# Optimization experiments

Hardware: AMD Instinct MI355X
Metric: run time of the kernel (lower is better)

Reference implementation:

```python
import jax, jax.numpy as jnp
import numpy as np

T = 16  # fixed number of timesteps in the original module


def _lin(k, out_d, in_d):
    kw, kb = jax.random.split(k)
    s = 1.0 / np.sqrt(in_d)
    W = jax.random.uniform(kw, (out_d, in_d), minval=-s, maxval=s, dtype=jnp.float32)
    b = jax.random.uniform(kb, (out_d,), minval=-s, maxval=s, dtype=jnp.float32)
    return W, b


def setup_inputs() -> dict:
    key = jax.random.key(0)
    B = 8192
    k = jax.random.split(key, 16)
    x = jax.random.normal(k[0], (T, B, 64), dtype=jnp.float32)
    cue = jax.random.uniform(k[1], (B,), dtype=jnp.float32)
    hc1 = jnp.zeros((B, 256), jnp.float32)
    hc2 = jnp.zeros((B, 256), jnp.float32)
    hc3 = jnp.zeros((B, 256), jnp.float32)
    hc4 = jnp.zeros((B, 64), jnp.float32)
    W1i, b1i = _lin(k[2], 256, 64)
    W1h, b1h = _lin(k[3], 256, 256)
    Wf1, bf1 = _lin(k[4], 256, 64)
    W1o, b1o = _lin(k[5], 64, 256)
    W2i, b2i = _lin(k[6], 256, 64)
    W2h, b2h = _lin(k[7], 256, 256)
    Wf2, bf2 = _lin(k[8], 256, 64)
    W2o, b2o = _lin(k[9], 64, 256)
    W3i, b3i = _lin(k[10], 256, 130)
    W3h, b3h = _lin(k[11], 256, 256)
    W3o, b3o = _lin(k[12], 64, 256)
    Wfc, bfc = _lin(k[13], 2, 64)
    return dict(x=x, cue=cue, hc1=hc1, hc2=hc2, hc3=hc3, hc4=hc4,
                W1i=W1i, b1i=b1i, W1h=W1h, b1h=b1h, Wf1=Wf1, bf1=bf1, W1o=W1o, b1o=b1o,
                W2i=W2i, b2i=b2i, W2h=W2h, b2h=b2h, Wf2=Wf2, bf2=bf2, W2o=W2o, b2o=b2o,
                W3i=W3i, b3i=b3i, W3h=W3h, b3h=b3h, W3o=W3o, b3o=b3o, Wfc=Wfc, bfc=bfc)


def reference(x, cue, hc1, hc2, hc3, hc4,
              W1i, b1i, W1h, b1h, Wf1, bf1, W1o, b1o,
              W2i, b2i, W2h, b2h, Wf2, bf2, W2o, b2o,
              W3i, b3i, W3h, b3h, W3o, b3o, Wfc, bfc):
    B = x.shape[1]
    # cue row is the same at every timestep: [B, 2]
    cue_row = jnp.stack([cue * 10.0, 10.0 * jnp.abs(cue - 1.0)], axis=-1)

    def step(carry, xi):
        h1, h2, h3, h4 = carry
        # RNN stack 1 with feedback from hc4
        feed1 = h4 @ Wf1.T + bf1                                    # [B,256] (pre-tanh, stored)
        h1n = jnp.tanh(xi @ W1i.T + b1i + h1 @ W1h.T + b1h + jnp.tanh(feed1))
        out1 = jnp.tanh(h1n @ W1o.T + b1o)                           # [B,64]
        # RNN stack 2 with feedback from hc4
        feed2 = h4 @ Wf2.T + bf2
        h2n = jnp.tanh(xi @ W2i.T + b2i + h2 @ W2h.T + b2h + jnp.tanh(feed2))
        out2 = jnp.tanh(h2n @ W2o.T + b2o)                           # [B,64]
        # RNN stack 3 over concat(cue, out1, out2): [B,130]
        mid = jnp.concatenate([cue_row, out1, out2], axis=-1)
        h3n = jnp.tanh(mid @ W3i.T + b3i + h3 @ W3h.T + b3h)
        o = h3n @ W3o.T + b3o                                        # [B,64]; becomes next hc4
        of = jax.nn.relu(o)
        outf = of @ Wfc.T + bfc                                      # [B,2]
        return (h1n, h2n, h3n, o), (outf, out1, out2, feed1, feed2, of)

    (h1, h2, h3, h4), (oseq, o1, o2, f1, f2, ofa) = jax.lax.scan(
        step, (hc1, hc2, hc3, hc4), x)
    cue_arr = jnp.broadcast_to(cue_row[None, :, :], (T, B, 2))
    return (oseq, h1, h2, h3, h4, o1, o2, cue_arr, f1, f2, ofa)
```

## Files before the change

kernel.cpp:

```cpp
#include <hip/hip_runtime.h>

typedef unsigned short ushort_t;
typedef __attribute__((ext_vector_type(8))) __bf16 bf8v;
typedef __attribute__((ext_vector_type(4))) float f4v;
typedef __attribute__((ext_vector_type(4))) unsigned short us4v;

#define MFMA(a, b, c) __builtin_amdgcn_mfma_f32_16x16x32_bf16((a), (b), (c), 0, 0, 0)

#define B_TOT 8192
#define T_STEPS 16
#define M_TILE 32
#define LDH 264
#define LDS_SM 72
#define LDMID 168

#define OW1I 0
#define OW1H 16384
#define OWF1 81920
#define OW1O 98304
#define OW2I 114688
#define OW2H 131072
#define OWF2 196608
#define OW2O 212992
#define OW3I 229376
#define OW3H 270336
#define OW3O 335872
#define OWFC 352256
#define WS_TOTAL 353280

#define O_OSEQ 0
#define O_H1   262144
#define O_H2   2359296
#define O_H3   4456448
#define O_H4   6553600
#define O_O1   7077888
#define O_O2   15466496
#define O_CUE  23855104
#define O_F1   24117248
#define O_F2   57671680
#define O_OFA  91226112

__device__ __forceinline__ ushort_t f2bf(float f) {
  union { float f; unsigned u; } v; v.f = f;
  unsigned r = v.u + 0x7fffu + ((v.u >> 16) & 1u);
  return (ushort_t)(r >> 16);
}

__device__ __forceinline__ float fast_tanh(float x) {
  float e = __expf(2.0f * x);
  return 1.0f - 2.0f * __builtin_amdgcn_rcpf(e + 1.0f);
}

__device__ __forceinline__ void store_bf4(ushort_t* p, f4v v) {
  us4v q;
  q[0] = f2bf(v[0]); q[1] = f2bf(v[1]); q[2] = f2bf(v[2]); q[3] = f2bf(v[3]);
  *(us4v*)p = q;
}

__global__ void prep_kernel(const float* __restrict__ W1i, const float* __restrict__ W1h,
                            const float* __restrict__ Wf1, const float* __restrict__ W1o,
                            const float* __restrict__ W2i, const float* __restrict__ W2h,
                            const float* __restrict__ Wf2, const float* __restrict__ W2o,
                            const float* __restrict__ W3i, const float* __restrict__ W3h,
                            const float* __restrict__ W3o, const float* __restrict__ Wfc,
                            ushort_t* __restrict__ ws) {
  int i = blockIdx.x * blockDim.x + threadIdx.x;
  if (i >= WS_TOTAL) return;
  float v;
  if (i < OW1H)       v = W1i[i - OW1I];
  else if (i < OWF1)  v = W1h[i - OW1H];
  else if (i < OW1O)  v = Wf1[i - OWF1];
  else if (i < OW2I)  v = W1o[i - OW1O];
  else if (i < OW2H)  v = W2i[i - OW2I];
  else if (i < OWF2)  v = W2h[i - OW2H];
  else if (i < OW2O)  v = Wf2[i - OWF2];
  else if (i < OW3I)  v = W2o[i - OW2O];
  else if (i < OW3H) {
    int idx = i - OW3I; int j = idx / 160; int k = idx - j * 160;
    if (k < 64)       v = W3i[j * 130 + 2 + k];
    else if (k < 128) v = W3i[j * 130 + 66 + (k - 64)];
    else if (k < 130) v = W3i[j * 130 + (k - 128)];
    else              v = 0.0f;
  }
  else if (i < OW3O)  v = W3h[i - OW3H];
  else if (i < OWFC)  v = W3o[i - OW3O];
  else {
    int idx = i - OWFC; int j = idx / 64; int k = idx - j * 64;
    v = (j < 2) ? Wfc[j * 64 + k] : 0.0f;
  }
  ws[i] = f2bf(v);
}

__launch_bounds__(512)
__global__ void rnn_kernel(const float* __restrict__ x, const float* __restrict__ cue,
                           const float* __restrict__ hc1, const float* __restrict__ hc2,
                           const float* __restrict__ hc3, const float* __restrict__ hc4,
                           const float* __restrict__ b1i, const float* __restrict__ b1h,
                           const float* __restrict__ bf1p, const float* __restrict__ b1o,
                           const float* __restrict__ b2i, const float* __restrict__ b2h,
                           const float* __restrict__ bf2p, const float* __restrict__ b2o,
                           const float* __restrict__ b3i, const float* __restrict__ b3h,
                           const float* __restrict__ b3o, const float* __restrict__ bfc,
                           const ushort_t* __restrict__ ws, float* __restrict__ out) {
  __shared__ ushort_t hs1[M_TILE * LDH], hs2[M_TILE * LDH], hs3[M_TILE * LDH];
  __shared__ ushort_t h4s[M_TILE * LDS_SM], xs[M_TILE * LDS_SM], ofs[M_TILE * LDS_SM];
  __shared__ ushort_t mid[M_TILE * LDMID];

  const int tid  = threadIdx.x;
  const int m0   = blockIdx.x * M_TILE;
  const int lane = tid & 63;
  const int w    = tid >> 6;
  const int ln   = lane & 15;
  const int quad = lane >> 4;
  const int koff = quad * 8;
  const int jt0  = 2 * w;

  for (int i = tid; i < M_TILE * 256; i += 512) {
    int m = i >> 8, j = i & 255;
    hs1[m * LDH + j] = f2bf(hc1[(m0 + m) * 256 + j]);
    hs2[m * LDH + j] = f2bf(hc2[(m0 + m) * 256 + j]);
    hs3[m * LDH + j] = f2bf(hc3[(m0 + m) * 256 + j]);
  }
  for (int i = tid; i < M_TILE * 64; i += 512) {
    int m = i >> 6, j = i & 63;
    h4s[m * LDS_SM + j] = f2bf(hc4[(m0 + m) * 64 + j]);
  }
  for (int i = tid; i < M_TILE * LDMID; i += 512) mid[i] = 0;
  {
    int t = tid >> 5, r = tid & 31;
    float c = cue[m0 + r];
    float* oc = out + O_CUE + ((size_t)t * B_TOT + m0 + r) * 2;
    oc[0] = c * 10.0f;
    oc[1] = 10.0f * fabsf(c - 1.0f);
  }
  __syncthreads();
  if (tid < M_TILE) {
    float c = cue[m0 + tid];
    mid[tid * LDMID + 128] = f2bf(c * 10.0f);
    mid[tid * LDMID + 129] = f2bf(10.0f * fabsf(c - 1.0f));
  }

  f4v bf1v[2], bf2v[2], bih1v[2], bih2v[2], b3shv[2];
#pragma unroll
  for (int i = 0; i < 2; ++i) {
    int j0 = (jt0 + i) * 16 + quad * 4;
#pragma unroll
    for (int r = 0; r < 4; ++r) {
      bf1v[i][r]  = bf1p[j0 + r];
      bf2v[i][r]  = bf2p[j0 + r];
      bih1v[i][r] = b1i[j0 + r] + b1h[j0 + r];
      bih2v[i][r] = b2i[j0 + r] + b2h[j0 + r];
      b3shv[i][r] = b3i[j0 + r] + b3h[j0 + r];
    }
  }
  const int jto3 = w & 3;
  const int j0o3 = jto3 * 16 + quad * 4;
  const bool isOut2 = (w >= 4);
  f4v bo3v;
#pragma unroll
  for (int r = 0; r < 4; ++r) bo3v[r] = isOut2 ? b2o[j0o3 + r] : b1o[j0o3 + r];
  const int jto5 = w >> 1;
  const int j0o5 = jto5 * 16 + quad * 4;
  const int mo5  = (w & 1) * 16 + ln;
  f4v b3ov;
#pragma unroll
  for (int r = 0; r < 4; ++r) b3ov[r] = b3o[j0o5 + r];
  const float bfcv0 = bfc[0], bfcv1 = bfc[1];

  __syncthreads();

  f4v acc1[2][2], acc2[2][2], acc3[2][2];

  for (int t = 0; t < T_STEPS; ++t) {
    {
      int r = tid >> 4, c4 = (tid & 15) * 4;
      const float* xp = x + ((size_t)t * B_TOT + m0 + r) * 64 + c4;
      f4v xv = *(const f4v*)xp;
      store_bf4(&xs[r * LDS_SM + c4], xv);
    }
    {
      f4v aF1[2][2], aF2[2][2];
#pragma unroll
      for (int i = 0; i < 2; ++i) {
#pragma unroll
        for (int mt = 0; mt < 2; ++mt) { aF1[i][mt] = bf1v[i]; aF2[i][mt] = bf2v[i]; }
      }
#pragma unroll
      for (int kk = 0; kk < 64; kk += 32) {
        bf8v b0 = *(const bf8v*)&h4s[ln * LDS_SM + kk + koff];
        bf8v b1 = *(const bf8v*)&h4s[(16 + ln) * LDS_SM + kk + koff];
#pragma unroll
        for (int i = 0; i < 2; ++i) {
          const int ar = ((jt0 + i) * 16 + ln) * 64 + kk + koff;
          bf8v a1 = *(const bf8v*)&ws[OWF1 + ar];
          bf8v a2 = *(const bf8v*)&ws[OWF2 + ar];
          aF1[i][0] = MFMA(a1, b0, aF1[i][0]);
          aF1[i][1] = MFMA(a1, b1, aF1[i][1]);
          aF2[i][0] = MFMA(a2, b0, aF2[i][0]);
          aF2[i][1] = MFMA(a2, b1, aF2[i][1]);
        }
      }
#pragma unroll
      for (int i = 0; i < 2; ++i) {
#pragma unroll
        for (int mt = 0; mt < 2; ++mt) {
          int j0 = (jt0 + i) * 16 + quad * 4;
          int m  = mt * 16 + ln;
          size_t rowoff = ((size_t)t * B_TOT + m0 + m) * 256 + j0;
          *(f4v*)(out + O_F1 + rowoff) = aF1[i][mt];
          *(f4v*)(out + O_F2 + rowoff) = aF2[i][mt];
          f4v t1, t2;
#pragma unroll
          for (int r = 0; r < 4; ++r) {
            t1[r] = fast_tanh(aF1[i][mt][r]) + bih1v[i][r];
            t2[r] = fast_tanh(aF2[i][mt][r]) + bih2v[i][r];
          }
          acc1[i][mt] = t1; acc2[i][mt] = t2; acc3[i][mt] = b3shv[i];
        }
      }
    }
    __syncthreads();

#pragma unroll
    for (int kk = 0; kk < 64; kk += 32) {
      bf8v b0 = *(const bf8v*)&xs[ln * LDS_SM + kk + koff];
      bf8v b1 = *(const bf8v*)&xs[(16 + ln) * LDS_SM + kk + koff];
#pragma unroll
      for (int i = 0; i < 2; ++i) {
        const int ar = ((jt0 + i) * 16 + ln) * 64 + kk + koff;
        bf8v a1 = *(const bf8v*)&ws[OW1I + ar];
        bf8v a2 = *(const bf8v*)&ws[OW2I + ar];
        acc1[i][0] = MFMA(a1, b0, acc1[i][0]);
        acc1[i][1] = MFMA(a1, b1, acc1[i][1]);
        acc2[i][0] = MFMA(a2, b0, acc2[i][0]);
        acc2[i][1] = MFMA(a2, b1, acc2[i][1]);
      }
    }
#pragma unroll
    for (int kk = 0; kk < 256; kk += 32) {
      bf8v q1a = *(const bf8v*)&hs1[ln * LDH + kk + koff];
      bf8v q1b = *(const bf8v*)&hs1[(16 + ln) * LDH + kk + koff];
      bf8v q2a = *(const bf8v*)&hs2[ln * LDH + kk + koff];
      bf8v q2b = *(const bf8v*)&hs2[(16 + ln) * LDH + kk + koff];
      bf8v q3a = *(const bf8v*)&hs3[ln * LDH + kk + koff];
      bf8v q3b = *(const bf8v*)&hs3[(16 + ln) * LDH + kk + koff];
#pragma unroll
      for (int i = 0; i < 2; ++i) {
        const int ar = ((jt0 + i) * 16 + ln) * 256 + kk + koff;
        bf8v a1 = *(const bf8v*)&ws[OW1H + ar];
        bf8v a2 = *(const bf8v*)&ws[OW2H + ar];
        bf8v a3 = *(const bf8v*)&ws[OW3H + ar];
        acc1[i][0] = MFMA(a1, q1a, acc1[i][0]);
        acc1[i][1] = MFMA(a1, q1b, acc1[i][1]);
        acc2[i][0] = MFMA(a2, q2a, acc2[i][0]);
        acc2[i][1] = MFMA(a2, q2b, acc2[i][1]);
        acc3[i][0] = MFMA(a3, q3a, acc3[i][0]);
        acc3[i][1] = MFMA(a3, q3b, acc3[i][1]);
      }
    }
#pragma unroll
    for (int i = 0; i < 2; ++i) {
#pragma unroll
      for (int mt = 0; mt < 2; ++mt) {
#pragma unroll
        for (int r = 0; r < 4; ++r) {
          acc1[i][mt][r] = fast_tanh(acc1[i][mt][r]);
          acc2[i][mt][r] = fast_tanh(acc2[i][mt][r]);
        }
      }
    }
    if (t == T_STEPS - 1) {
#pragma unroll
      for (int i = 0; i < 2; ++i) {
#pragma unroll
        for (int mt = 0; mt < 2; ++mt) {
          int j0 = (jt0 + i) * 16 + quad * 4;
          int m  = mt * 16 + ln;
          *(f4v*)(out + O_H1 + (size_t)(m0 + m) * 256 + j0) = acc1[i][mt];
          *(f4v*)(out + O_H2 + (size_t)(m0 + m) * 256 + j0) = acc2[i][mt];
        }
      }
    }
    __syncthreads();

#pragma unroll
    for (int i = 0; i < 2; ++i) {
#pragma unroll
      for (int mt = 0; mt < 2; ++mt) {
        int j0 = (jt0 + i) * 16 + quad * 4;
        int m  = mt * 16 + ln;
        store_bf4(&hs1[m * LDH + j0], acc1[i][mt]);
        store_bf4(&hs2[m * LDH + j0], acc2[i][mt]);
      }
    }
    __syncthreads();

    {
      const ushort_t* hsrc = isOut2 ? hs2 : hs1;
      const int wbase = isOut2 ? OW2O : OW1O;
      f4v aO[2];
      aO[0] = bo3v; aO[1] = bo3v;
#pragma unroll
      for (int kk = 0; kk < 256; kk += 32) {
        bf8v b0 = *(const bf8v*)&hsrc[ln * LDH + kk + koff];
        bf8v b1 = *(const bf8v*)&hsrc[(16 + ln) * LDH + kk + koff];
        bf8v a  = *(const bf8v*)&ws[wbase + (jto3 * 16 + ln) * 256 + kk + koff];
        aO[0] = MFMA(a, b0, aO[0]);
        aO[1] = MFMA(a, b1, aO[1]);
      }
#pragma unroll
      for (int mt = 0; mt < 2; ++mt) {
#pragma unroll
        for (int r = 0; r < 4; ++r) aO[mt][r] = fast_tanh(aO[mt][r]);
        int m = mt * 16 + ln;
        size_t ob = ((size_t)t * B_TOT + m0 + m) * 64 + j0o3;
        *(f4v*)(out + (isOut2 ? O_O2 : O_O1) + ob) = aO[mt];
        store_bf4(&mid[m * LDMID + (isOut2 ? 64 : 0) + j0o3], aO[mt]);
      }
    }
    __syncthreads();

#pragma unroll
    for (int kk = 0; kk < 160; kk += 32) {
      bf8v b0 = *(const bf8v*)&mid[ln * LDMID + kk + koff];
      bf8v b1 = *(const bf8v*)&mid[(16 + ln) * LDMID + kk + koff];
#pragma unroll
      for (int i = 0; i < 2; ++i) {
        bf8v a = *(const bf8v*)&ws[OW3I + ((jt0 + i) * 16 + ln) * 160 + kk + koff];
        acc3[i][0] = MFMA(a, b0, acc3[i][0]);
        acc3[i][1] = MFMA(a, b1, acc3[i][1]);
      }
    }
#pragma unroll
    for (int i = 0; i < 2; ++i) {
#pragma unroll
      for (int mt = 0; mt < 2; ++mt) {
#pragma unroll
        for (int r = 0; r < 4; ++r) acc3[i][mt][r] = fast_tanh(acc3[i][mt][r]);
        int j0 = (jt0 + i) * 16 + quad * 4;
        int m  = mt * 16 + ln;
        if (t == T_STEPS - 1)
          *(f4v*)(out + O_H3 + (size_t)(m0 + m) * 256 + j0) = acc3[i][mt];
        store_bf4(&hs3[m * LDH + j0], acc3[i][mt]);
      }
    }
    __syncthreads();

    {
      f4v aO = b3ov;
#pragma unroll
      for (int kk = 0; kk < 256; kk += 32) {
        bf8v b = *(const bf8v*)&hs3[mo5 * LDH + kk + koff];
        bf8v a = *(const bf8v*)&ws[OW3O + (jto5 * 16 + ln) * 256 + kk + koff];
        aO = MFMA(a, b, aO);
      }
      store_bf4(&h4s[mo5 * LDS_SM + j0o5], aO);
      if (t == T_STEPS - 1)
        *(f4v*)(out + O_H4 + (size_t)(m0 + mo5) * 64 + j0o5) = aO;
      f4v rl;
#pragma unroll
      for (int r = 0; r < 4; ++r) rl[r] = fmaxf(aO[r], 0.0f);
      *(f4v*)(out + O_OFA + ((size_t)t * B_TOT + m0 + mo5) * 64 + j0o5) = rl;
      store_bf4(&ofs[mo5 * LDS_SM + j0o5], rl);
    }
    __syncthreads();

    if (w < 2) {
      f4v aFc;
      aFc[0] = (quad == 0) ? bfcv0 : 0.0f;
      aFc[1] = (quad == 0) ? bfcv1 : 0.0f;
      aFc[2] = 0.0f; aFc[3] = 0.0f;
#pragma unroll
      for (int kk = 0; kk < 64; kk += 32) {
        bf8v b = *(const bf8v*)&ofs[(w * 16 + ln) * LDS_SM + kk + koff];
        bf8v a = *(const bf8v*)&ws[OWFC + ln * 64 + kk + koff];
        aFc = MFMA(a, b, aFc);
      }
      if (quad == 0) {
        float* po = out + O_OSEQ + ((size_t)t * B_TOT + m0 + w * 16 + ln) * 2;
        po[0] = aFc[0];
        po[1] = aFc[1];
      }
    }
  }
}

extern "C" void kernel_launch(void* const* d_in, const int* in_sizes, int n_in,
                              void* d_out, int out_size, void* d_ws, size_t ws_size,
                              hipStream_t stream) {
  const float* x   = (const float*)d_in[0];
  const float* cue = (const float*)d_in[1];
  const float* hc1 = (const float*)d_in[2];
  const float* hc2 = (const float*)d_in[3];
  const float* hc3 = (const float*)d_in[4];
  const float* hc4 = (const float*)d_in[5];
  const float* W1i = (const float*)d_in[6];
  const float* b1i = (const float*)d_in[7];
  const float* W1h = (const float*)d_in[8];
  const float* b1h = (const float*)d_in[9];
  const float* Wf1 = (const float*)d_in[10];
  const float* bf1 = (const float*)d_in[11];
  const float* W1o = (const float*)d_in[12];
  const float* b1o = (const float*)d_in[13];
  const float* W2i = (const float*)d_in[14];
  const float* b2i = (const float*)d_in[15];
  const float* W2h = (const float*)d_in[16];
  const float* b2h = (const float*)d_in[17];
  const float* Wf2 = (const float*)d_in[18];
  const float* bf2 = (const float*)d_in[19];
  const float* W2o = (const float*)d_in[20];
  const float* b2o = (const float*)d_in[21];
  const float* W3i = (const float*)d_in[22];
  const float* b3i = (const float*)d_in[23];
  const float* W3h = (const float*)d_in[24];
  const float* b3h = (const float*)d_in[25];
  const float* W3o = (const float*)d_in[26];
  const float* b3o = (const float*)d_in[27];
  const float* Wfc = (const float*)d_in[28];
  const float* bfc = (const float*)d_in[29];

  ushort_t* ws = (ushort_t*)d_ws;
  float* out = (float*)d_out;

  prep_kernel<<<(WS_TOTAL + 511) / 512, 512, 0, stream>>>(
      W1i, W1h, Wf1, W1o, W2i, W2h, Wf2, W2o, W3i, W3h, W3o, Wfc, ws);

  rnn_kernel<<<B_TOT / M_TILE, 512, 0, stream>>>(
      x, cue, hc1, hc2, hc3, hc4,
      b1i, b1h, bf1, b1o, b2i, b2h, bf2, b2o, b3i, b3h, b3o, bfc,
      ws, out);
}
```

Before: 960.8 us.

## Halve batch tile to 16 rows per block and use nontemporal global stores

Cuts the per-block batch tile from 32 to 16 rows, which doubles the grid to 512 blocks and drops the second M-subtile from every MFMA loop. Launch bounds now ask for 4 blocks per CU, and initial-state loads are vectorized. Streaming outputs and x loads switch to nontemporal builtins. The goal is more blocks and better latency hiding on a serial recurrence, but each weight fragment is now reused across half as many rows, so weight traffic from L2 per output roughly doubles.

```diff
diff --git a/kernel.cpp b/kernel.cpp
--- a/kernel.cpp
+++ b/kernel.cpp
@@ -9,7 +9,7 @@
 
 #define B_TOT 8192
 #define T_STEPS 16
-#define M_TILE 32
+#define M_TILE 16
 #define LDH 264
 #define LDS_SM 72
 #define LDMID 168
@@ -55,6 +55,13 @@
   us4v q;
   q[0] = f2bf(v[0]); q[1] = f2bf(v[1]); q[2] = f2bf(v[2]); q[3] = f2bf(v[3]);
   *(us4v*)p = q;
+}
+
+__device__ __forceinline__ void nt_st4(float* p, f4v v) {
+  __builtin_nontemporal_store(v, (f4v*)p);
+}
+__device__ __forceinline__ f4v nt_ld4(const float* p) {
+  return __builtin_nontemporal_load((const f4v*)p);
 }
 
 __global__ void prep_kernel(const float* __restrict__ W1i, const float* __restrict__ W1h,
@@ -91,7 +98,7 @@
   ws[i] = f2bf(v);
 }
 
-__launch_bounds__(512)
+__launch_bounds__(512, 4)
 __global__ void rnn_kernel(const float* __restrict__ x, const float* __restrict__ cue,
                            const float* __restrict__ hc1, const float* __restrict__ hc2,
                            const float* __restrict__ hc3, const float* __restrict__ hc4,
@@ -115,23 +122,23 @@
   const int koff = quad * 8;
   const int jt0  = 2 * w;
 
-  for (int i = tid; i < M_TILE * 256; i += 512) {
-    int m = i >> 8, j = i & 255;
-    hs1[m * LDH + j] = f2bf(hc1[(m0 + m) * 256 + j]);
-    hs2[m * LDH + j] = f2bf(hc2[(m0 + m) * 256 + j]);
-    hs3[m * LDH + j] = f2bf(hc3[(m0 + m) * 256 + j]);
-  }
   for (int i = tid; i < M_TILE * 64; i += 512) {
-    int m = i >> 6, j = i & 63;
-    h4s[m * LDS_SM + j] = f2bf(hc4[(m0 + m) * 64 + j]);
+    int m = i >> 6, j4 = (i & 63) * 4;
+    store_bf4(&hs1[m * LDH + j4], nt_ld4(&hc1[(size_t)(m0 + m) * 256 + j4]));
+    store_bf4(&hs2[m * LDH + j4], nt_ld4(&hc2[(size_t)(m0 + m) * 256 + j4]));
+    store_bf4(&hs3[m * LDH + j4], nt_ld4(&hc3[(size_t)(m0 + m) * 256 + j4]));
+  }
+  if (tid < M_TILE * 16) {
+    int m = tid >> 4, j4 = (tid & 15) * 4;
+    store_bf4(&h4s[m * LDS_SM + j4], nt_ld4(&hc4[(size_t)(m0 + m) * 64 + j4]));
   }
   for (int i = tid; i < M_TILE * LDMID; i += 512) mid[i] = 0;
-  {
-    int t = tid >> 5, r = tid & 31;
+  if (tid < 256) {
+    int t = tid >> 4, r = tid & 15;
     float c = cue[m0 + r];
     float* oc = out + O_CUE + ((size_t)t * B_TOT + m0 + r) * 2;
-    oc[0] = c * 10.0f;
-    oc[1] = 10.0f * fabsf(c - 1.0f);
+    __builtin_nontemporal_store(c * 10.0f, oc);
+    __builtin_nontemporal_store(10.0f * fabsf(c - 1.0f), oc + 1);
   }
   __syncthreads();
   if (tid < M_TILE) {
@@ -159,9 +166,8 @@
   f4v bo3v;
 #pragma unroll
   for (int r = 0; r < 4; ++r) bo3v[r] = isOut2 ? b2o[j0o3 + r] : b1o[j0o3 + r];
-  const int jto5 = w >> 1;
+  const int jto5 = w & 3;
   const int j0o5 = jto5 * 16 + quad * 4;
-  const int mo5  = (w & 1) * 16 + ln;
   f4v b3ov;
 #pragma unroll
   for (int r = 0; r < 4; ++r) b3ov[r] = b3o[j0o5 + r];
@@ -169,54 +175,43 @@
 
   __syncthreads();
 
-  f4v acc1[2][2], acc2[2][2], acc3[2][2];
+  f4v acc1[2], acc2[2], acc3[2];
 
   for (int t = 0; t < T_STEPS; ++t) {
-    {
+    if (tid < 256) {
       int r = tid >> 4, c4 = (tid & 15) * 4;
       const float* xp = x + ((size_t)t * B_TOT + m0 + r) * 64 + c4;
-      f4v xv = *(const f4v*)xp;
-      store_bf4(&xs[r * LDS_SM + c4], xv);
+      store_bf4(&xs[r * LDS_SM + c4], nt_ld4(xp));
     }
     {
-      f4v aF1[2][2], aF2[2][2];
-#pragma unroll
-      for (int i = 0; i < 2; ++i) {
-#pragma unroll
-        for (int mt = 0; mt < 2; ++mt) { aF1[i][mt] = bf1v[i]; aF2[i][mt] = bf2v[i]; }
-      }
+      f4v aF1[2], aF2[2];
+#pragma unroll
+      for (int i = 0; i < 2; ++i) { aF1[i] = bf1v[i]; aF2[i] = bf2v[i]; }
 #pragma unroll
       for (int kk = 0; kk < 64; kk += 32) {
         bf8v b0 = *(const bf8v*)&h4s[ln * LDS_SM + kk + koff];
-        bf8v b1 = *(const bf8v*)&h4s[(16 + ln) * LDS_SM + kk + koff];
 #pragma unroll
         for (int i = 0; i < 2; ++i) {
           const int ar = ((jt0 + i) * 16 + ln) * 64 + kk + koff;
           bf8v a1 = *(const bf8v*)&ws[OWF1 + ar];
           bf8v a2 = *(const bf8v*)&ws[OWF2 + ar];
-          aF1[i][0] = MFMA(a1, b0, aF1[i][0]);
-          aF1[i][1] = MFMA(a1, b1, aF1[i][1]);
-          aF2[i][0] = MFMA(a2, b0, aF2[i][0]);
-          aF2[i][1] = MFMA(a2, b1, aF2[i][1]);
+          aF1[i] = MFMA(a1, b0, aF1[i]);
+          aF2[i] = MFMA(a2, b0, aF2[i]);
         }
       }
 #pragma unroll
       for (int i = 0; i < 2; ++i) {
-#pragma unroll
-        for (int mt = 0; mt < 2; ++mt) {
-          int j0 = (jt0 + i) * 16 + quad * 4;
-          int m  = mt * 16 + ln;
-          size_t rowoff = ((size_t)t * B_TOT + m0 + m) * 256 + j0;
-          *(f4v*)(out + O_F1 + rowoff) = aF1[i][mt];
-          *(f4v*)(out + O_F2 + rowoff) = aF2[i][mt];
-          f4v t1, t2;
-#pragma unroll
-          for (int r = 0; r < 4; ++r) {
-            t1[r] = fast_tanh(aF1[i][mt][r]) + bih1v[i][r];
-            t2[r] = fast_tanh(aF2[i][mt][r]) + bih2v[i][r];
-          }
-          acc1[i][mt] = t1; acc2[i][mt] = t2; acc3[i][mt] = b3shv[i];
+        int j0 = (jt0 + i) * 16 + quad * 4;
+        size_t rowoff = ((size_t)t * B_TOT + m0 + ln) * 256 + j0;
+        nt_st4(out + O_F1 + rowoff, aF1[i]);
+        nt_st4(out + O_F2 + rowoff, aF2[i]);
+        f4v t1, t2;
+#pragma unroll
+        for (int r = 0; r < 4; ++r) {
+          t1[r] = fast_tanh(aF1[i][r]) + bih1v[i][r];
+          t2[r] = fast_tanh(aF2[i][r]) + bih2v[i][r];
         }
+        acc1[i] = t1; acc2[i] = t2; acc3[i] = b3shv[i];
       }
     }
     __syncthreads();
@@ -224,162 +219,129 @@
 #pragma unroll
     for (int kk = 0; kk < 64; kk += 32) {
       bf8v b0 = *(const bf8v*)&xs[ln * LDS_SM + kk + koff];
-      bf8v b1 = *(const bf8v*)&xs[(16 + ln) * LDS_SM + kk + koff];
 #pragma unroll
       for (int i = 0; i < 2; ++i) {
         const int ar = ((jt0 + i) * 16 + ln) * 64 + kk + koff;
         bf8v a1 = *(const bf8v*)&ws[OW1I + ar];
         bf8v a2 = *(const bf8v*)&ws[OW2I + ar];
-        acc1[i][0] = MFMA(a1, b0, acc1[i][0]);
-        acc1[i][1] = MFMA(a1, b1, acc1[i][1]);
-        acc2[i][0] = MFMA(a2, b0, acc2[i][0]);
-        acc2[i][1] = MFMA(a2, b1, acc2[i][1]);
+        acc1[i] = MFMA(a1, b0, acc1[i]);
+        acc2[i] = MFMA(a2, b0, acc2[i]);
       }
     }
 #pragma unroll
     for (int kk = 0; kk < 256; kk += 32) {
-      bf8v q1a = *(const bf8v*)&hs1[ln * LDH + kk + koff];
-      bf8v q1b = *(const bf8v*)&hs1[(16 + ln) * LDH + kk + koff];
-      bf8v q2a = *(const bf8v*)&hs2[ln * LDH + kk + koff];
-      bf8v q2b = *(const bf8v*)&hs2[(16 + ln) * LDH + kk + koff];
-      bf8v q3a = *(const bf8v*)&hs3[ln * LDH + kk + koff];
-      bf8v q3b = *(const bf8v*)&hs3[(16 + ln) * LDH + kk + koff];
+      bf8v q1 = *(const bf8v*)&hs1[ln * LDH + kk + koff];
+      bf8v q2 = *(const bf8v*)&hs2[ln * LDH + kk + koff];
+      bf8v q3 = *(const bf8v*)&hs3[ln * LDH + kk + koff];
 #pragma unroll
       for (int i = 0; i < 2; ++i) {
         const int ar = ((jt0 + i) * 16 + ln) * 256 + kk + koff;
         bf8v a1 = *(const bf8v*)&ws[OW1H + ar];
         bf8v a2 = *(const bf8v*)&ws[OW2H + ar];
         bf8v a3 = *(const bf8v*)&ws[OW3H + ar];
-        acc1[i][0] = MFMA(a1, q1a, acc1[i][0]);
-        acc1[i][1] = MFMA(a1, q1b, acc1[i][1]);
-        acc2[i][0] = MFMA(a2, q2a, acc2[i][0]);
-        acc2[i][1] = MFMA(a2, q2b, acc2[i][1]);
-        acc3[i][0] = MFMA(a3, q3a, acc3[i][0]);
-        acc3[i][1] = MFMA(a3, q3b, acc3[i][1]);
+        acc1[i] = MFMA(a1, q1, acc1[i]);
+        acc2[i] = MFMA(a2, q2, acc2[i]);
+        acc3[i] = MFMA(a3, q3, acc3[i]);
       }
     }
 #pragma unroll
     for (int i = 0; i < 2; ++i) {
 #pragma unroll
-      for (int mt = 0; mt < 2; ++mt) {
-#pragma unroll
-        for (int r = 0; r < 4; ++r) {
-          acc1[i][mt][r] = fast_tanh(acc1[i][mt][r]);
-          acc2[i][mt][r] = fast_tanh(acc2[i][mt][r]);
-        }
+      for (int r = 0; r < 4; ++r) {
+        acc1[i][r] = fast_tanh(acc1[i][r]);
+        acc2[i][r] = fast_tanh(acc2[i][r]);
       }
     }
     if (t == T_STEPS - 1) {
 #pragma unroll
       for (int i = 0; i < 2; ++i) {
-#pragma unroll
-        for (int mt = 0; mt < 2; ++mt) {
-          int j0 = (jt0 + i) * 16 + quad * 4;
-          int m  = mt * 16 + ln;
-          *(f4v*)(out + O_H1 + (size_t)(m0 + m) * 256 + j0) = acc1[i][mt];
-          *(f4v*)(out + O_H2 + (size_t)(m0 + m) * 256 + j0) = acc2[i][mt];
-        }
+        int j0 = (jt0 + i) * 16 + quad * 4;
+        *(f4v*)(out + O_H1 + (size_t)(m0 + ln) * 256 + j0) = acc1[i];
+        *(f4v*)(out + O_H2 + (size_t)(m0 + ln) * 256 + j0) = acc2[i];
       }
     }
     __syncthreads();
 
 #pragma unroll
     for (int i = 0; i < 2; ++i) {
-#pragma unroll
-      for (int mt = 0; mt < 2; ++mt) {
-        int j0 = (jt0 + i) * 16 + quad * 4;
-        int m  = mt * 16 + ln;
-        store_bf4(&hs1[m * LDH + j0], acc1[i][mt]);
-        store_bf4(&hs2[m * LDH + j0], acc2[i][mt]);
-      }
+      int j0 = (jt0 + i) * 16 + quad * 4;
+      store_bf4(&hs1[ln * LDH + j0], acc1[i]);
+      store_bf4(&hs2[ln * LDH + j0], acc2[i]);
     }
     __syncthreads();
 
     {
       const ushort_t* hsrc = isOut2 ? hs2 : hs1;
       const int wbase = isOut2 ? OW2O : OW1O;
-      f4v aO[2];
-      aO[0] = bo3v; aO[1] = bo3v;
+      f4v aO = bo3v;
 #pragma unroll
       for (int kk = 0; kk < 256; kk += 32) {
         bf8v b0 = *(const bf8v*)&hsrc[ln * LDH + kk + koff];
-        bf8v b1 = *(const bf8v*)&hsrc[(16 + ln) * LDH + kk + koff];
         bf8v a  = *(const bf8v*)&ws[wbase + (jto3 * 16 + ln) * 256 + kk + koff];
-        aO[0] = MFMA(a, b0, aO[0]);
-        aO[1] = MFMA(a, b1, aO[1]);
-      }
-#pragma unroll
-      for (int mt = 0; mt < 2; ++mt) {
-#pragma unroll
-        for (int r = 0; r < 4; ++r) aO[mt][r] = fast_tanh(aO[mt][r]);
-        int m = mt * 16 + ln;
-        size_t ob = ((size_t)t * B_TOT + m0 + m) * 64 + j0o3;
-        *(f4v*)(out + (isOut2 ? O_O2 : O_O1) + ob) = aO[mt];
-        store_bf4(&mid[m * LDMID + (isOut2 ? 64 : 0) + j0o3], aO[mt]);
-      }
+        aO = MFMA(a, b0, aO);
+      }
+#pragma unroll
+      for (int r = 0; r < 4; ++r) aO[r] = fast_tanh(aO[r]);
+      size_t ob = ((size_t)t * B_TOT + m0 + ln) * 64 + j0o3;
+      nt_st4(out + (isOut2 ? O_O2 : O_O1) + ob, aO);
+      store_bf4(&mid[ln * LDMID + (isOut2 ? 64 : 0) + j0o3], aO);
     }
     __syncthreads();
 
 #pragma unroll
     for (int kk = 0; kk < 160; kk += 32) {
       bf8v b0 = *(const bf8v*)&mid[ln * LDMID + kk + koff];
-      bf8v b1 = *(const bf8v*)&mid[(16 + ln) * LDMID + kk + koff];
 #pragma unroll
       for (int i = 0; i < 2; ++i) {
         bf8v a = *(const bf8v*)&ws[OW3I + ((jt0 + i) * 16 + ln) * 160 + kk + koff];
-        acc3[i][0] = MFMA(a, b0, acc3[i][0]);
-        acc3[i][1] = MFMA(a, b1, acc3[i][1]);
+        acc3[i] = MFMA(a, b0, acc3[i]);
       }
     }
 #pragma unroll
     for (int i = 0; i < 2; ++i) {
 #pragma unroll
-      for (int mt = 0; mt < 2; ++mt) {
-#pragma unroll
-        for (int r = 0; r < 4; ++r) acc3[i][mt][r] = fast_tanh(acc3[i][mt][r]);
-        int j0 = (jt0 + i) * 16 + quad * 4;
-        int m  = mt * 16 + ln;
-        if (t == T_STEPS - 1)
-          *(f4v*)(out + O_H3 + (size_t)(m0 + m) * 256 + j0) = acc3[i][mt];
-        store_bf4(&hs3[m * LDH + j0], acc3[i][mt]);
-      }
-    }
-    __syncthreads();
-
-    {
+      for (int r = 0; r < 4; ++r) acc3[i][r] = fast_tanh(acc3[i][r]);
+      int j0 = (jt0 + i) * 16 + quad * 4;
+      if (t == T_STEPS - 1)
+        *(f4v*)(out + O_H3 + (size_t)(m0 + ln) * 256 + j0) = acc3[i];
+      store_bf4(&hs3[ln * LDH + j0], acc3[i]);
+    }
+    __syncthreads();
+
+    if (w < 4) {
       f4v aO = b3ov;
 #pragma unroll
       for (int kk = 0; kk < 256; kk += 32) {
-        bf8v b = *(const bf8v*)&hs3[mo5 * LDH + kk + koff];
+        bf8v b = *(const bf8v*)&hs3[ln * LDH + kk + koff];
         bf8v a = *(const bf8v*)&ws[OW3O + (jto5 * 16 + ln) * 256 + kk + koff];
         aO = MFMA(a, b, aO);
       }
-      store_bf4(&h4s[mo5 * LDS_SM + j0o5], aO);
+      store_bf4(&h4s[ln * LDS_SM + j0o5], aO);
       if (t == T_STEPS - 1)
-        *(f4v*)(out + O_H4 + (size_t)(m0 + mo5) * 64 + j0o5) = aO;
+        *(f4v*)(out + O_H4 + (size_t)(m0 + ln) * 64 + j0o5) = aO;
       f4v rl;
 #pragma unroll
       for (int r = 0; r < 4; ++r) rl[r] = fmaxf(aO[r], 0.0f);
-      *(f4v*)(out + O_OFA + ((size_t)t * B_TOT + m0 + mo5) * 64 + j0o5) = rl;
-      store_bf4(&ofs[mo5 * LDS_SM + j0o5], rl);
-    }
-    __syncthreads();
-
-    if (w < 2) {
+      nt_st4(out + O_OFA + ((size_t)t * B_TOT + m0 + ln) * 64 + j0o5, rl);
+      store_bf4(&ofs[ln * LDS_SM + j0o5], rl);
+    }
+    __syncthreads();
+
+    if (w == 0) {
       f4v aFc;
       aFc[0] = (quad == 0) ? bfcv0 : 0.0f;
       aFc[1] = (quad == 0) ? bfcv1 : 0.0f;
       aFc[2] = 0.0f; aFc[3] = 0.0f;
 #pragma unroll
       for (int kk = 0; kk < 64; kk += 32) {
-        bf8v b = *(const bf8v*)&ofs[(w * 16 + ln) * LDS_SM + kk + koff];
+        bf8v b = *(const bf8v*)&ofs[ln * LDS_SM + kk + koff];
         bf8v a = *(const bf8v*)&ws[OWFC + ln * 64 + kk + koff];
         aFc = MFMA(a, b, aFc);
       }
       if (quad == 0) {
-        float* po = out + O_OSEQ + ((size_t)t * B_TOT + m0 + w * 16 + ln) * 2;
-        po[0] = aFc[0];
-        po[1] = aFc[1];
+        float* po = out + O_OSEQ + ((size_t)t * B_TOT + m0 + ln) * 2;
+        __builtin_nontemporal_store(aFc[0], po);
+        __builtin_nontemporal_store(aFc[1], po + 1);
       }
     }
   }
```

Measured after the change: 1.695 ms. +76.5%, slower.
